# Performance work log

Measured on AMD Instinct MI355X. Metric: run time of the kernel, lower is better.

## Reference

```python
import jax, jax.numpy as jnp
import numpy as np

B, S, D, H, O = 4, 128, 768, 768, 2

def setup_inputs() -> dict:
    key = jax.random.key(0)
    ks = jax.random.split(key, 6)
    scale = 1.0 / np.sqrt(2 * D)
    return {
        "a": jax.random.normal(ks[0], (B, S, D), jnp.float32),
        "b": jax.random.normal(ks[1], (B, S, D), jnp.float32),
        "W1": jax.random.normal(ks[2], (2 * D, H), jnp.float32) * scale,
        "b1": jax.random.normal(ks[3], (H,), jnp.float32) * 0.01,
        "W2": jax.random.normal(ks[4], (H, O), jnp.float32) * (1.0 / np.sqrt(H)),
        "b2": jax.random.normal(ks[5], (O,), jnp.float32) * 0.01,
    }

def reference(a, b, W1, b1, W2, b2):
    # Pairwise concat [a_i ; b_j] followed by Linear(2D->H) is algebraically
    # identical to projecting a and b separately and broadcast-adding
    # (biaffine-style rewrite; same math as cat+matmul, less HBM traffic).
    d = a.shape[-1]
    ha = jnp.einsum('bsd,dh->bsh', a, W1[:d])        # (B, Sa, H)
    hb = jnp.einsum('btd,dh->bth', b, W1[d:])        # (B, Sb, H)
    h = jax.nn.relu(ha[:, :, None, :] + hb[:, None, :, :] + b1)  # (B, Sa, Sb, H)
    scores = jnp.einsum('bsth,ho->bsto', h, W2) + b2  # (B, Sa, Sb, O)
    return scores
```

## Files before the change

### kernel.cpp

```cpp
#include <hip/hip_runtime.h>
#include <hip/hip_bf16.h>


typedef __attribute__((ext_vector_type(8))) short short8;
typedef __attribute__((ext_vector_type(4))) float floatx4;
typedef unsigned int uint;

__device__ __forceinline__ short f2bf(float f) {
    __hip_bfloat16 h = __float2bfloat16(f);
    short s; __builtin_memcpy(&s, &h, 2); return s;
}
__device__ __forceinline__ float bflo(uint u) {
    uint v = u << 16; float f; __builtin_memcpy(&f, &v, 4); return f;
}
__device__ __forceinline__ float bfhi(uint u) {
    uint v = u & 0xffff0000u; float f; __builtin_memcpy(&f, &v, 4); return f;
}

__global__ __launch_bounds__(256) void init_out_kernel(
    const float* __restrict__ b2, float* __restrict__ out)
{
    const float w0 = b2[0], w1 = b2[1];
    const float4 v = make_float4(w0, w1, w0, w1);
    const int base = blockIdx.x * 2048 + threadIdx.x * 8;
    *(float4*)&out[base]     = v;
    *(float4*)&out[base + 4] = v;
}

__global__ __launch_bounds__(256) void gemm_kernel(
    const float* __restrict__ a, const float* __restrict__ bmat,
    const float* __restrict__ W1, const float* __restrict__ b1,
    ushort* __restrict__ Hbf)
{
    const int which = blockIdx.z;
    const int n0 = blockIdx.x * 64;
    const int m0 = blockIdx.y * 64;
    const int t  = threadIdx.x;

    __shared__ ushort As[64][40];
    __shared__ ushort Bs[64][40];

    const int srow = t >> 2;
    const int skc  = (t & 3) * 8;
    const float* __restrict__ Asrc = which ? bmat : a;
    const float* __restrict__ aptr = Asrc + (size_t)(m0 + srow) * 768 + skc;

    const int ncolS = t & 63;
    const int kg0   = (t >> 6) * 8;
    const float* __restrict__ bptr = W1 + (size_t)(which * 768 + kg0) * 768 + n0 + ncolS;

    float4 af0 = *(const float4*)(aptr);
    float4 af1 = *(const float4*)(aptr + 4);
    float breg[8];
#pragma unroll
    for (int j = 0; j < 8; j++) breg[j] = bptr[(size_t)j * 768];

    const int lane = t & 63;
    const int w    = t >> 6;
    const int lr   = lane & 15;
    const int lq   = lane >> 4;

    floatx4 acc0 = {0,0,0,0}, acc1 = {0,0,0,0}, acc2 = {0,0,0,0}, acc3 = {0,0,0,0};

    for (int kt = 0; kt < 768; kt += 32) {
        __syncthreads();
        short8 ap;
        ap[0]=f2bf(af0.x); ap[1]=f2bf(af0.y); ap[2]=f2bf(af0.z); ap[3]=f2bf(af0.w);
        ap[4]=f2bf(af1.x); ap[5]=f2bf(af1.y); ap[6]=f2bf(af1.z); ap[7]=f2bf(af1.w);
        *(short8*)&As[srow][skc] = ap;
        short8 bp;
        bp[0]=f2bf(breg[0]); bp[1]=f2bf(breg[1]); bp[2]=f2bf(breg[2]); bp[3]=f2bf(breg[3]);
        bp[4]=f2bf(breg[4]); bp[5]=f2bf(breg[5]); bp[6]=f2bf(breg[6]); bp[7]=f2bf(breg[7]);
        *(short8*)&Bs[ncolS][kg0] = bp;
        __syncthreads();

        if (kt + 32 < 768) {
            af0 = *(const float4*)(aptr + kt + 32);
            af1 = *(const float4*)(aptr + kt + 36);
#pragma unroll
            for (int j = 0; j < 8; j++) breg[j] = bptr[(size_t)(kt + 32 + j) * 768];
        }

        short8 bfr = *(const short8*)&Bs[w * 16 + lr][lq * 8];
        short8 a0  = *(const short8*)&As[     lr][lq * 8];
        short8 a1  = *(const short8*)&As[16 + lr][lq * 8];
        short8 a2  = *(const short8*)&As[32 + lr][lq * 8];
        short8 a3  = *(const short8*)&As[48 + lr][lq * 8];
        acc0 = __builtin_amdgcn_mfma_f32_16x16x32_bf16(a0, bfr, acc0, 0, 0, 0);
        acc1 = __builtin_amdgcn_mfma_f32_16x16x32_bf16(a1, bfr, acc1, 0, 0, 0);
        acc2 = __builtin_amdgcn_mfma_f32_16x16x32_bf16(a2, bfr, acc2, 0, 0, 0);
        acc3 = __builtin_amdgcn_mfma_f32_16x16x32_bf16(a3, bfr, acc3, 0, 0, 0);
    }

    const int ncol = n0 + w * 16 + lr;
    const float bias = which ? 0.f : b1[ncol];
    ushort* __restrict__ dst = Hbf + (size_t)which * 393216 + ncol;
    const int rbase = m0 + lq * 4;
#pragma unroll
    for (int r = 0; r < 4; r++) {
        dst[(size_t)(rbase +      r) * 768] = (ushort)f2bf(acc0[r] + bias);
        dst[(size_t)(rbase + 16 + r) * 768] = (ushort)f2bf(acc1[r] + bias);
        dst[(size_t)(rbase + 32 + r) * 768] = (ushort)f2bf(acc2[r] + bias);
        dst[(size_t)(rbase + 48 + r) * 768] = (ushort)f2bf(acc3[r] + bias);
    }
}

__global__ __launch_bounds__(256) void pair_kernel(
    const ushort* __restrict__ Hbf, const float* __restrict__ W2,
    float* __restrict__ out)
{
    const int bb = blockIdx.z >> 2;
    const int hc = blockIdx.z & 3;
    const int s0 = blockIdx.y * 32;
    const int t0 = blockIdx.x * 32;
    const int tid = threadIdx.x;

    __shared__ ushort hAs[32][200];
    __shared__ ushort hBs[32][200];
    __shared__ __align__(16) float w2s[384];

    const int hbase = hc * 192;
    const ushort* __restrict__ Asrc = Hbf +          (size_t)(bb * 128 + s0) * 768 + hbase;
    const ushort* __restrict__ Bsrc = Hbf + 393216 + (size_t)(bb * 128 + t0) * 768 + hbase;

#pragma unroll
    for (int i = 0; i < 3; i++) {
        const int c   = tid + i * 256;
        const int row = c / 24;
        const int c16 = c % 24;
        *(uint4*)&hAs[row][c16 * 8] = *(const uint4*)(Asrc + (size_t)row * 768 + c16 * 8);
        *(uint4*)&hBs[row][c16 * 8] = *(const uint4*)(Bsrc + (size_t)row * 768 + c16 * 8);
    }
    if (tid < 96) *(float4*)&w2s[tid * 4] = *(const float4*)&W2[hbase * 2 + tid * 4];
    __syncthreads();

    const int tl = tid & 15;
    const int sl = tid >> 4;

    float acc[2][2][2] = {};

    for (int h8 = 0; h8 < 192; h8 += 8) {
        const uint4 ra0 = *(const uint4*)&hAs[2 * sl    ][h8];
        const uint4 ra1 = *(const uint4*)&hAs[2 * sl + 1][h8];
        const uint4 rb0 = *(const uint4*)&hBs[2 * tl    ][h8];
        const uint4 rb1 = *(const uint4*)&hBs[2 * tl + 1][h8];
        const uint a0d[4] = {ra0.x, ra0.y, ra0.z, ra0.w};
        const uint a1d[4] = {ra1.x, ra1.y, ra1.z, ra1.w};
        const uint b0d[4] = {rb0.x, rb0.y, rb0.z, rb0.w};
        const uint b1d[4] = {rb1.x, rb1.y, rb1.z, rb1.w};
#pragma unroll
        for (int d = 0; d < 4; d++) {
            const float4 wv = *(const float4*)&w2s[h8 * 2 + d * 4];
            {
                const float a0 = bflo(a0d[d]), a1 = bflo(a1d[d]);
                const float b0 = bflo(b0d[d]), b1 = bflo(b1d[d]);
                float h;
                h = fmaxf(a0 + b0, 0.f); acc[0][0][0] = fmaf(h, wv.x, acc[0][0][0]); acc[0][0][1] = fmaf(h, wv.y, acc[0][0][1]);
                h = fmaxf(a0 + b1, 0.f); acc[0][1][0] = fmaf(h, wv.x, acc[0][1][0]); acc[0][1][1] = fmaf(h, wv.y, acc[0][1][1]);
                h = fmaxf(a1 + b0, 0.f); acc[1][0][0] = fmaf(h, wv.x, acc[1][0][0]); acc[1][0][1] = fmaf(h, wv.y, acc[1][0][1]);
                h = fmaxf(a1 + b1, 0.f); acc[1][1][0] = fmaf(h, wv.x, acc[1][1][0]); acc[1][1][1] = fmaf(h, wv.y, acc[1][1][1]);
            }
            {
                const float a0 = bfhi(a0d[d]), a1 = bfhi(a1d[d]);
                const float b0 = bfhi(b0d[d]), b1 = bfhi(b1d[d]);
                float h;
                h = fmaxf(a0 + b0, 0.f); acc[0][0][0] = fmaf(h, wv.z, acc[0][0][0]); acc[0][0][1] = fmaf(h, wv.w, acc[0][0][1]);
                h = fmaxf(a0 + b1, 0.f); acc[0][1][0] = fmaf(h, wv.z, acc[0][1][0]); acc[0][1][1] = fmaf(h, wv.w, acc[0][1][1]);
                h = fmaxf(a1 + b0, 0.f); acc[1][0][0] = fmaf(h, wv.z, acc[1][0][0]); acc[1][0][1] = fmaf(h, wv.w, acc[1][0][1]);
                h = fmaxf(a1 + b1, 0.f); acc[1][1][0] = fmaf(h, wv.z, acc[1][1][0]); acc[1][1][1] = fmaf(h, wv.w, acc[1][1][1]);
            }
        }
    }

    const int sg = bb * 128 + s0 + 2 * sl;
    const int tg = t0 + 2 * tl;
    float* ob = out + (size_t)sg * 256 + tg * 2;
    atomicAdd(ob + 0,   acc[0][0][0]); atomicAdd(ob + 1,   acc[0][0][1]);
    atomicAdd(ob + 2,   acc[0][1][0]); atomicAdd(ob + 3,   acc[0][1][1]);
    atomicAdd(ob + 256, acc[1][0][0]); atomicAdd(ob + 257, acc[1][0][1]);
    atomicAdd(ob + 258, acc[1][1][0]); atomicAdd(ob + 259, acc[1][1][1]);
}

extern "C" void kernel_launch(void* const* d_in, const int* in_sizes, int n_in,
                              void* d_out, int out_size, void* d_ws, size_t ws_size,
                              hipStream_t stream) {
    const float* a  = (const float*)d_in[0];
    const float* b  = (const float*)d_in[1];
    const float* W1 = (const float*)d_in[2];
    const float* b1 = (const float*)d_in[3];
    const float* W2 = (const float*)d_in[4];
    const float* b2 = (const float*)d_in[5];
    float* out = (float*)d_out;

    ushort* Hbf = (ushort*)d_ws;

    init_out_kernel<<<64, 256, 0, stream>>>(b2, out);
    gemm_kernel<<<dim3(12, 8, 2), 256, 0, stream>>>(a, b, W1, b1, Hbf);
    pair_kernel<<<dim3(4, 4, 16), 256, 0, stream>>>(Hbf, W2, out);
}
```

Baseline: 98.55 us.

## Switch to fp16 packed math with dot2 in pair kernel, drop atomics and init

Stores the intermediate projections in fp16 instead of bf16, converting with packed round-toward-zero and using fp16 MFMA in the projection GEMM. The pairwise kernel now does add and ReLU as packed half2 ops and accumulates with fdot2 against fp16-packed W2, which roughly halves the VALU instruction count per pair. Each block now covers the full hidden dimension for a 16x16 tile, so it writes its output directly with the bias added, removing the init kernel and the atomics. This risks fp16 range and rounding error in the ReLU sums and gives each block a longer serial loop with fewer outputs per thread.

```diff
diff --git a/kernel.cpp b/kernel.cpp
--- a/kernel.cpp
+++ b/kernel.cpp
@@ -1,36 +1,21 @@
 #include <hip/hip_runtime.h>
-#include <hip/hip_bf16.h>
+#include <hip/hip_fp16.h>
 
 
-typedef __attribute__((ext_vector_type(8))) short short8;
+typedef __attribute__((ext_vector_type(2))) _Float16 half2t;
+typedef __attribute__((ext_vector_type(8))) _Float16 half8t;
 typedef __attribute__((ext_vector_type(4))) float floatx4;
 typedef unsigned int uint;
 
-__device__ __forceinline__ short f2bf(float f) {
-    __hip_bfloat16 h = __float2bfloat16(f);
-    short s; __builtin_memcpy(&s, &h, 2); return s;
-}
-__device__ __forceinline__ float bflo(uint u) {
-    uint v = u << 16; float f; __builtin_memcpy(&f, &v, 4); return f;
-}
-__device__ __forceinline__ float bfhi(uint u) {
-    uint v = u & 0xffff0000u; float f; __builtin_memcpy(&f, &v, 4); return f;
-}
-
-__global__ __launch_bounds__(256) void init_out_kernel(
-    const float* __restrict__ b2, float* __restrict__ out)
-{
-    const float w0 = b2[0], w1 = b2[1];
-    const float4 v = make_float4(w0, w1, w0, w1);
-    const int base = blockIdx.x * 2048 + threadIdx.x * 8;
-    *(float4*)&out[base]     = v;
-    *(float4*)&out[base + 4] = v;
+__device__ __forceinline__ half2t pkrtz(float x, float y) {
+    __fp16 r __attribute__((ext_vector_type(2))) = __builtin_amdgcn_cvt_pkrtz(x, y);
+    half2t o; __builtin_memcpy(&o, &r, 4); return o;
 }
 
 __global__ __launch_bounds__(256) void gemm_kernel(
     const float* __restrict__ a, const float* __restrict__ bmat,
     const float* __restrict__ W1, const float* __restrict__ b1,
-    ushort* __restrict__ Hbf)
+    ushort* __restrict__ Hf)
 {
     const int which = blockIdx.z;
     const int n0 = blockIdx.x * 64;
@@ -64,14 +49,18 @@
 
     for (int kt = 0; kt < 768; kt += 32) {
         __syncthreads();
-        short8 ap;
-        ap[0]=f2bf(af0.x); ap[1]=f2bf(af0.y); ap[2]=f2bf(af0.z); ap[3]=f2bf(af0.w);
-        ap[4]=f2bf(af1.x); ap[5]=f2bf(af1.y); ap[6]=f2bf(af1.z); ap[7]=f2bf(af1.w);
-        *(short8*)&As[srow][skc] = ap;
-        short8 bp;
-        bp[0]=f2bf(breg[0]); bp[1]=f2bf(breg[1]); bp[2]=f2bf(breg[2]); bp[3]=f2bf(breg[3]);
-        bp[4]=f2bf(breg[4]); bp[5]=f2bf(breg[5]); bp[6]=f2bf(breg[6]); bp[7]=f2bf(breg[7]);
-        *(short8*)&Bs[ncolS][kg0] = bp;
+        half2t ap[4];
+        ap[0] = pkrtz(af0.x, af0.y);
+        ap[1] = pkrtz(af0.z, af0.w);
+        ap[2] = pkrtz(af1.x, af1.y);
+        ap[3] = pkrtz(af1.z, af1.w);
+        __builtin_memcpy(&As[srow][skc], ap, 16);
+        half2t bp[4];
+        bp[0] = pkrtz(breg[0], breg[1]);
+        bp[1] = pkrtz(breg[2], breg[3]);
+        bp[2] = pkrtz(breg[4], breg[5]);
+        bp[3] = pkrtz(breg[6], breg[7]);
+        __builtin_memcpy(&Bs[ncolS][kg0], bp, 16);
         __syncthreads();
 
         if (kt + 32 < 768) {
@@ -81,104 +70,100 @@
             for (int j = 0; j < 8; j++) breg[j] = bptr[(size_t)(kt + 32 + j) * 768];
         }
 
-        short8 bfr = *(const short8*)&Bs[w * 16 + lr][lq * 8];
-        short8 a0  = *(const short8*)&As[     lr][lq * 8];
-        short8 a1  = *(const short8*)&As[16 + lr][lq * 8];
-        short8 a2  = *(const short8*)&As[32 + lr][lq * 8];
-        short8 a3  = *(const short8*)&As[48 + lr][lq * 8];
-        acc0 = __builtin_amdgcn_mfma_f32_16x16x32_bf16(a0, bfr, acc0, 0, 0, 0);
-        acc1 = __builtin_amdgcn_mfma_f32_16x16x32_bf16(a1, bfr, acc1, 0, 0, 0);
-        acc2 = __builtin_amdgcn_mfma_f32_16x16x32_bf16(a2, bfr, acc2, 0, 0, 0);
-        acc3 = __builtin_amdgcn_mfma_f32_16x16x32_bf16(a3, bfr, acc3, 0, 0, 0);
+        half8t bfr, a0, a1, a2, a3;
+        __builtin_memcpy(&bfr, &Bs[w * 16 + lr][lq * 8], 16);
+        __builtin_memcpy(&a0,  &As[     lr][lq * 8], 16);
+        __builtin_memcpy(&a1,  &As[16 + lr][lq * 8], 16);
+        __builtin_memcpy(&a2,  &As[32 + lr][lq * 8], 16);
+        __builtin_memcpy(&a3,  &As[48 + lr][lq * 8], 16);
+        acc0 = __builtin_amdgcn_mfma_f32_16x16x32_f16(a0, bfr, acc0, 0, 0, 0);
+        acc1 = __builtin_amdgcn_mfma_f32_16x16x32_f16(a1, bfr, acc1, 0, 0, 0);
+        acc2 = __builtin_amdgcn_mfma_f32_16x16x32_f16(a2, bfr, acc2, 0, 0, 0);
+        acc3 = __builtin_amdgcn_mfma_f32_16x16x32_f16(a3, bfr, acc3, 0, 0, 0);
     }
 
     const int ncol = n0 + w * 16 + lr;
     const float bias = which ? 0.f : b1[ncol];
-    ushort* __restrict__ dst = Hbf + (size_t)which * 393216 + ncol;
+    ushort* __restrict__ dst = Hf + (size_t)which * 393216 + ncol;
     const int rbase = m0 + lq * 4;
 #pragma unroll
     for (int r = 0; r < 4; r++) {
-        dst[(size_t)(rbase +      r) * 768] = (ushort)f2bf(acc0[r] + bias);
-        dst[(size_t)(rbase + 16 + r) * 768] = (ushort)f2bf(acc1[r] + bias);
-        dst[(size_t)(rbase + 32 + r) * 768] = (ushort)f2bf(acc2[r] + bias);
-        dst[(size_t)(rbase + 48 + r) * 768] = (ushort)f2bf(acc3[r] + bias);
+        _Float16 v0 = (_Float16)(acc0[r] + bias);
+        _Float16 v1 = (_Float16)(acc1[r] + bias);
+        _Float16 v2 = (_Float16)(acc2[r] + bias);
+        _Float16 v3 = (_Float16)(acc3[r] + bias);
+        ushort u0, u1, u2, u3;
+        __builtin_memcpy(&u0, &v0, 2); __builtin_memcpy(&u1, &v1, 2);
+        __builtin_memcpy(&u2, &v2, 2); __builtin_memcpy(&u3, &v3, 2);
+        dst[(size_t)(rbase +      r) * 768] = u0;
+        dst[(size_t)(rbase + 16 + r) * 768] = u1;
+        dst[(size_t)(rbase + 32 + r) * 768] = u2;
+        dst[(size_t)(rbase + 48 + r) * 768] = u3;
     }
 }
 
 __global__ __launch_bounds__(256) void pair_kernel(
-    const ushort* __restrict__ Hbf, const float* __restrict__ W2,
-    float* __restrict__ out)
+    const ushort* __restrict__ Hf, const float* __restrict__ W2,
+    const float* __restrict__ b2, float* __restrict__ out)
 {
-    const int bb = blockIdx.z >> 2;
-    const int hc = blockIdx.z & 3;
-    const int s0 = blockIdx.y * 32;
-    const int t0 = blockIdx.x * 32;
+    const int bb = blockIdx.z;
+    const int s0 = blockIdx.y * 16;
+    const int t0 = blockIdx.x * 16;
     const int tid = threadIdx.x;
 
-    __shared__ ushort hAs[32][200];
-    __shared__ ushort hBs[32][200];
-    __shared__ __align__(16) float w2s[384];
+    __shared__ ushort hAs[16][776];
+    __shared__ ushort hBs[16][776];
+    __shared__ uint w2s[768];
 
-    const int hbase = hc * 192;
-    const ushort* __restrict__ Asrc = Hbf +          (size_t)(bb * 128 + s0) * 768 + hbase;
-    const ushort* __restrict__ Bsrc = Hbf + 393216 + (size_t)(bb * 128 + t0) * 768 + hbase;
+    const ushort* __restrict__ Asrc = Hf +          (size_t)(bb * 128 + s0) * 768;
+    const ushort* __restrict__ Bsrc = Hf + 393216 + (size_t)(bb * 128 + t0) * 768;
 
 #pragma unroll
-    for (int i = 0; i < 3; i++) {
+    for (int i = 0; i < 6; i++) {
         const int c   = tid + i * 256;
-        const int row = c / 24;
-        const int c16 = c % 24;
-        *(uint4*)&hAs[row][c16 * 8] = *(const uint4*)(Asrc + (size_t)row * 768 + c16 * 8);
-        *(uint4*)&hBs[row][c16 * 8] = *(const uint4*)(Bsrc + (size_t)row * 768 + c16 * 8);
+        const int row = c / 96;
+        const int col = (c % 96) * 8;
+        *(uint4*)&hAs[row][col] = *(const uint4*)(Asrc + (size_t)row * 768 + col);
+        *(uint4*)&hBs[row][col] = *(const uint4*)(Bsrc + (size_t)row * 768 + col);
     }
-    if (tid < 96) *(float4*)&w2s[tid * 4] = *(const float4*)&W2[hbase * 2 + tid * 4];
+#pragma unroll
+    for (int j = tid; j < 768; j += 256) {
+        const int o  = (j >= 384) ? 1 : 0;
+        const int h2 = j - o * 384;
+        half2t p = pkrtz(W2[4 * h2 + o], W2[4 * h2 + 2 + o]);
+        uint u; __builtin_memcpy(&u, &p, 4);
+        w2s[j] = u;
+    }
     __syncthreads();
 
+    const int sl = tid >> 4;
     const int tl = tid & 15;
-    const int sl = tid >> 4;
+    const ushort* __restrict__ arow = &hAs[sl][0];
+    const ushort* __restrict__ brow = &hBs[tl][0];
 
-    float acc[2][2][2] = {};
+    float acc0 = 0.f, acc1 = 0.f;
+    const half2t zero = {(_Float16)0.f, (_Float16)0.f};
 
-    for (int h8 = 0; h8 < 192; h8 += 8) {
-        const uint4 ra0 = *(const uint4*)&hAs[2 * sl    ][h8];
-        const uint4 ra1 = *(const uint4*)&hAs[2 * sl + 1][h8];
-        const uint4 rb0 = *(const uint4*)&hBs[2 * tl    ][h8];
-        const uint4 rb1 = *(const uint4*)&hBs[2 * tl + 1][h8];
-        const uint a0d[4] = {ra0.x, ra0.y, ra0.z, ra0.w};
-        const uint a1d[4] = {ra1.x, ra1.y, ra1.z, ra1.w};
-        const uint b0d[4] = {rb0.x, rb0.y, rb0.z, rb0.w};
-        const uint b1d[4] = {rb1.x, rb1.y, rb1.z, rb1.w};
+#pragma unroll 8
+    for (int h8 = 0; h8 < 768; h8 += 8) {
+        half2t pa[4], pb[4], w0[4], w1[4];
+        __builtin_memcpy(pa, arow + h8, 16);
+        __builtin_memcpy(pb, brow + h8, 16);
+        __builtin_memcpy(w0, &w2s[h8 / 2], 16);
+        __builtin_memcpy(w1, &w2s[384 + h8 / 2], 16);
 #pragma unroll
-        for (int d = 0; d < 4; d++) {
-            const float4 wv = *(const float4*)&w2s[h8 * 2 + d * 4];
-            {
-                const float a0 = bflo(a0d[d]), a1 = bflo(a1d[d]);
-                const float b0 = bflo(b0d[d]), b1 = bflo(b1d[d]);
-                float h;
-                h = fmaxf(a0 + b0, 0.f); acc[0][0][0] = fmaf(h, wv.x, acc[0][0][0]); acc[0][0][1] = fmaf(h, wv.y, acc[0][0][1]);
-                h = fmaxf(a0 + b1, 0.f); acc[0][1][0] = fmaf(h, wv.x, acc[0][1][0]); acc[0][1][1] = fmaf(h, wv.y, acc[0][1][1]);
-                h = fmaxf(a1 + b0, 0.f); acc[1][0][0] = fmaf(h, wv.x, acc[1][0][0]); acc[1][0][1] = fmaf(h, wv.y, acc[1][0][1]);
-                h = fmaxf(a1 + b1, 0.f); acc[1][1][0] = fmaf(h, wv.x, acc[1][1][0]); acc[1][1][1] = fmaf(h, wv.y, acc[1][1][1]);
-            }
-            {
-                const float a0 = bfhi(a0d[d]), a1 = bfhi(a1d[d]);
-                const float b0 = bfhi(b0d[d]), b1 = bfhi(b1d[d]);
-                float h;
-                h = fmaxf(a0 + b0, 0.f); acc[0][0][0] = fmaf(h, wv.z, acc[0][0][0]); acc[0][0][1] = fmaf(h, wv.w, acc[0][0][1]);
-                h = fmaxf(a0 + b1, 0.f); acc[0][1][0] = fmaf(h, wv.z, acc[0][1][0]); acc[0][1][1] = fmaf(h, wv.w, acc[0][1][1]);
-                h = fmaxf(a1 + b0, 0.f); acc[1][0][0] = fmaf(h, wv.z, acc[1][0][0]); acc[1][0][1] = fmaf(h, wv.w, acc[1][0][1]);
-                h = fmaxf(a1 + b1, 0.f); acc[1][1][0] = fmaf(h, wv.z, acc[1][1][0]); acc[1][1][1] = fmaf(h, wv.w, acc[1][1][1]);
-            }
+        for (int j = 0; j < 4; j++) {
+            half2t s = pa[j] + pb[j];
+            s = __builtin_elementwise_max(s, zero);
+            acc0 = __builtin_amdgcn_fdot2(s, w0[j], acc0, false);
+            acc1 = __builtin_amdgcn_fdot2(s, w1[j], acc1, false);
         }
     }
 
-    const int sg = bb * 128 + s0 + 2 * sl;
-    const int tg = t0 + 2 * tl;
-    float* ob = out + (size_t)sg * 256 + tg * 2;
-    atomicAdd(ob + 0,   acc[0][0][0]); atomicAdd(ob + 1,   acc[0][0][1]);
-    atomicAdd(ob + 2,   acc[0][1][0]); atomicAdd(ob + 3,   acc[0][1][1]);
-    atomicAdd(ob + 256, acc[1][0][0]); atomicAdd(ob + 257, acc[1][0][1]);
-    atomicAdd(ob + 258, acc[1][1][0]); atomicAdd(ob + 259, acc[1][1][1]);
+    const int sg = bb * 128 + s0 + sl;
+    const int tg = t0 + tl;
+    float2 r = make_float2(acc0 + b2[0], acc1 + b2[1]);
+    *(float2*)&out[((size_t)sg * 128 + tg) * 2] = r;
 }
 
 extern "C" void kernel_launch(void* const* d_in, const int* in_sizes, int n_in,
@@ -192,9 +177,8 @@
     const float* b2 = (const float*)d_in[5];
     float* out = (float*)d_out;
 
-    ushort* Hbf = (ushort*)d_ws;
+    ushort* Hf = (ushort*)d_ws;
 
-    init_out_kernel<<<64, 256, 0, stream>>>(b2, out);
-    gemm_kernel<<<dim3(12, 8, 2), 256, 0, stream>>>(a, b, W1, b1, Hbf);
-    pair_kernel<<<dim3(4, 4, 16), 256, 0, stream>>>(Hbf, W2, out);
+    gemm_kernel<<<dim3(12, 8, 2), 256, 0, stream>>>(a, b, W1, b1, Hf);
+    pair_kernel<<<dim3(8, 8, 4), 256, 0, stream>>>(Hf, W2, b2, out);
 }
```

Result: faster. 89.06 us (-9.6%).
